# Optimization experiments

Hardware: AMD Instinct MI355X
Metric: run time of the kernel (lower is better)

The kernel has to match this reference:

```python
import jax, jax.numpy as jnp
import numpy as np

B, N, C, F, O = 32, 2048, 8, 128, 128


def setup_inputs() -> dict:
    key = jax.random.key(0)
    k1, k2, k3, k4, k5, k6 = jax.random.split(key, 6)
    nodes = jax.random.normal(k1, (B, N, F), dtype=jnp.float32)
    children = jax.random.randint(k2, (B, N, C), 0, N, dtype=jnp.int32)
    w_t = jax.random.normal(k3, (F, O), dtype=jnp.float32) * 0.05
    w_l = jax.random.normal(k4, (F, O), dtype=jnp.float32) * 0.05
    w_r = jax.random.normal(k5, (F, O), dtype=jnp.float32) * 0.05
    b = jax.random.normal(k6, (O,), dtype=jnp.float32) * 0.05
    return {"nodes": nodes, "children": children, "w_t": w_t, "w_l": w_l, "w_r": w_r, "b": b}


def reference(nodes, children, w_t, w_l, w_r, b):
    Bb, Nn, Ff = nodes.shape
    Cc = children.shape[2]
    dt = nodes.dtype

    # --- children tensor: index 0 maps to zero vector ---
    lookup = jnp.concatenate([jnp.zeros((Bb, 1, Ff), dt), nodes[:, 1:, :]], axis=1)
    batch_idx = jnp.arange(Bb)[:, None, None]
    child_vecs = lookup[batch_idx, children]                      # [B,N,C,F]
    tree = jnp.concatenate([nodes[:, :, None, :], child_vecs], axis=2)  # [B,N,C+1,F]

    # --- coefficients ---
    ch_f = children.astype(dt)
    c_t = jnp.broadcast_to(
        jnp.concatenate([jnp.ones((1, 1, 1), dt), jnp.zeros((1, 1, Cc), dt)], axis=2),
        (Bb, Nn, Cc + 1))                                          # [B,N,C+1]
    num_sib = jnp.count_nonzero(children, axis=2, keepdims=True).astype(dt)  # [B,N,1]
    mask = jnp.concatenate(
        [jnp.zeros((Bb, Nn, 1), dt), jnp.minimum(ch_f, 1.0)], axis=2)        # [B,N,C+1]
    child_indices = jnp.arange(-1.0, Cc, 1.0, dtype=dt)[None, None, :] * mask
    singles = jnp.concatenate(
        [jnp.zeros((Bb, Nn, 1), dt),
         jnp.full((Bb, Nn, 1), 0.5, dt),
         jnp.zeros((Bb, Nn, Cc - 1), dt)], axis=2)
    is_single = num_sib == 1.0
    denom = jnp.where(is_single, 1.0, num_sib - 1.0)  # safe divide, matches tf.where select
    c_r = jnp.where(is_single, singles, (1.0 - c_t) * (child_indices / denom))
    c_l = (1.0 - c_t) * (1.0 - c_r) * mask
    coef = jnp.stack([c_t, c_r, c_l], axis=3)                      # [B,N,C+1,3]

    # --- weighted aggregation + small GEMM ---
    agg = jnp.einsum('bncf,bnck->bnkf', tree, coef)                # [B,N,3,F]
    w = jnp.stack([w_t, w_r, w_l], axis=0)                         # [3,F,O]
    out = jnp.einsum('bnkf,kfo->bno', agg, w)
    return jax.nn.relu(out + b)
```

## Files before the change

kernel.cpp:

```cpp
#include <hip/hip_runtime.h>

typedef unsigned short ushort_t;
typedef __attribute__((ext_vector_type(8))) short short8;
typedef __attribute__((ext_vector_type(4))) float float4v;
typedef __attribute__((ext_vector_type(2))) unsigned int uint2v;

#define Bn 32
#define Nn 2048
#define Cn 8
#define Fn 128
#define On 128
#define Kn 384
#define MT 16
#define LDSK 392

__device__ __forceinline__ ushort_t f2bf(float x) {
  unsigned u = __float_as_uint(x);
  u += 0x7fffu + ((u >> 16) & 1u);
  return (ushort_t)(u >> 16);
}

__device__ __forceinline__ unsigned cvt_pk_bf16(float lo, float hi) {
  unsigned r;
  asm("v_cvt_pk_bf16_f32 %0, %1, %2" : "=v"(r) : "v"(lo), "v"(hi));
  return r;
}

__device__ __forceinline__ uint2v pack4(float4v v) {
  uint2v r;
  r.x = cvt_pk_bf16(v.x, v.y);
  r.y = cvt_pk_bf16(v.z, v.w);
  return r;
}

__global__ void prep_w_kernel(const float* __restrict__ w_t,
                              const float* __restrict__ w_l,
                              const float* __restrict__ w_r,
                              ushort_t* __restrict__ wsw) {
  int t = blockIdx.x * blockDim.x + threadIdx.x;
  if (t >= 6144) return;
  int lane = t & 63;
  int r = t >> 6;
  int ks = r % 12;
  int q = r / 12;
  int col = q * 16 + (lane & 15);
  int kbase = ((lane >> 4) * 8) + ks * 32;
  ushort_t* dst = wsw + (size_t)t * 8;
#pragma unroll
  for (int j = 0; j < 8; ++j) {
    int k = kbase + j;
    const float* src = (k < Fn) ? w_t : (k < 2 * Fn) ? w_r : w_l;
    int f = k & (Fn - 1);
    dst[j] = f2bf(src[f * On + col]);
  }
}

__device__ __forceinline__ void issue_row(const float* __restrict__ nodes,
                                          int sb, int grp, int ln,
                                          const int4& a, const int4& b,
                                          int it, float4v (&dst)[9]) {
  const int row = it * 4 + grp;
  const int g = sb * MT + row;
  const int base_row = g & ~(Nn - 1);
  const float4v* np = (const float4v*)nodes;
  dst[0] = np[(size_t)g * (Fn / 4) + ln];
  const int id[Cn] = {a.x, a.y, a.z, a.w, b.x, b.y, b.z, b.w};
#pragma unroll
  for (int c = 0; c < Cn; ++c) {
    const int ix = id[c] & (Nn - 1);
    dst[1 + c] = np[(size_t)(base_row + ix) * (Fn / 4) + ln];
  }
}

__device__ __forceinline__ void compute_row(ushort_t* __restrict__ agg,
                                            int grp, int ln,
                                            const int4& a, const int4& b,
                                            int it, const float4v (&v)[9]) {
  const int row = it * 4 + grp;
  const int id[Cn] = {a.x, a.y, a.z, a.w, b.x, b.y, b.z, b.w};
  int ns = 0;
#pragma unroll
  for (int c = 0; c < Cn; ++c) ns += (id[c] != 0) ? 1 : 0;
  const bool single = (ns == 1);
  const float rden = (ns > 1) ? (1.0f / (float)(ns - 1)) : 0.0f;

  float4v rr = {0.f, 0.f, 0.f, 0.f};
  float4v ms = {0.f, 0.f, 0.f, 0.f};
#pragma unroll
  for (int c = 0; c < Cn; ++c) {
    const float m = (id[c] != 0) ? 1.0f : 0.0f;
    float cr = single ? ((c == 0) ? 0.5f : 0.0f) : ((float)c * rden);
    cr *= m;
    const float4v vc = v[1 + c];
    rr += cr * vc;
    ms += m * vc;
  }
  const float4v ll = ms - rr;

  ushort_t* arow = agg + row * LDSK + ln * 4;
  *(uint2v*)(arow)           = pack4(v[0]);
  *(uint2v*)(arow + Fn)      = pack4(rr);
  *(uint2v*)(arow + 2 * Fn)  = pack4(ll);
}

__device__ __forceinline__ void store_ct(float* __restrict__ out,
                                         const float* __restrict__ bias,
                                         int sb, int l15, int quad, int q,
                                         const float4v& acc) {
  const int col = q * 16 + l15;
  const float bb = bias[col];
  const int grow0 = sb * MT + quad * 4;
#pragma unroll
  for (int r2 = 0; r2 < 4; ++r2) {
    out[(size_t)(grow0 + r2) * On + col] = fmaxf(acc[r2] + bb, 0.f);
  }
}

__global__ __launch_bounds__(128, 3)
void tree_conv_kernel(const float* __restrict__ nodes,
                      const int* __restrict__ children,
                      const ushort_t* __restrict__ wsw,
                      const float* __restrict__ bias,
                      float* __restrict__ out) {
  __shared__ __align__(16) ushort_t agg[MT * LDSK];

  const int tid = threadIdx.x;

  const int sb = ((blockIdx.x & 7) << 9) | (blockIdx.x >> 3);

  {
    const int grp = tid >> 5;
    const int ln = tid & 31;

    int4 ca[4], cb[4];
#pragma unroll
    for (int it = 0; it < 4; ++it) {
      const int g = sb * MT + it * 4 + grp;
      const int4* chv = (const int4*)(children + (size_t)g * Cn);
      ca[it] = chv[0];
      cb[it] = chv[1];
    }

    float4v v0[9], v1[9];
    issue_row(nodes, sb, grp, ln, ca[0], cb[0], 0, v0);
    issue_row(nodes, sb, grp, ln, ca[1], cb[1], 1, v1);
    compute_row(agg, grp, ln, ca[0], cb[0], 0, v0);
    issue_row(nodes, sb, grp, ln, ca[2], cb[2], 2, v0);
    compute_row(agg, grp, ln, ca[1], cb[1], 1, v1);
    issue_row(nodes, sb, grp, ln, ca[3], cb[3], 3, v1);
    compute_row(agg, grp, ln, ca[2], cb[2], 2, v0);
    compute_row(agg, grp, ln, ca[3], cb[3], 3, v1);
  }

  const int lane = tid & 63;
  const int wave = tid >> 6;
  const int l15 = lane & 15;
  const int quad = lane >> 4;

  short8 bf0[12], bf1[12];
  const short8* bbase = (const short8*)wsw + lane;
#pragma unroll
  for (int ks = 0; ks < 12; ++ks) bf0[ks] = bbase[((wave * 4 + 0) * 12 + ks) * 64];
#pragma unroll
  for (int ks = 0; ks < 12; ++ks) bf1[ks] = bbase[((wave * 4 + 1) * 12 + ks) * 64];

  asm volatile("s_waitcnt lgkmcnt(0)" ::: "memory");
  __builtin_amdgcn_s_barrier();
  asm volatile("" ::: "memory");

  const ushort_t* ar = agg + l15 * LDSK + quad * 8;
  short8 af[12];
#pragma unroll
  for (int ks = 0; ks < 12; ++ks) af[ks] = *(const short8*)(ar + ks * 32);

  float4v acc;

  acc = (float4v){0.f, 0.f, 0.f, 0.f};
#pragma unroll
  for (int ks = 0; ks < 12; ++ks)
    acc = __builtin_amdgcn_mfma_f32_16x16x32_bf16(af[ks], bf0[ks], acc, 0, 0, 0);
#pragma unroll
  for (int ks = 0; ks < 12; ++ks) bf0[ks] = bbase[((wave * 4 + 2) * 12 + ks) * 64];
  store_ct(out, bias, sb, l15, quad, wave * 4 + 0, acc);

  acc = (float4v){0.f, 0.f, 0.f, 0.f};
#pragma unroll
  for (int ks = 0; ks < 12; ++ks)
    acc = __builtin_amdgcn_mfma_f32_16x16x32_bf16(af[ks], bf1[ks], acc, 0, 0, 0);
#pragma unroll
  for (int ks = 0; ks < 12; ++ks) bf1[ks] = bbase[((wave * 4 + 3) * 12 + ks) * 64];
  store_ct(out, bias, sb, l15, quad, wave * 4 + 1, acc);

  acc = (float4v){0.f, 0.f, 0.f, 0.f};
#pragma unroll
  for (int ks = 0; ks < 12; ++ks)
    acc = __builtin_amdgcn_mfma_f32_16x16x32_bf16(af[ks], bf0[ks], acc, 0, 0, 0);
  store_ct(out, bias, sb, l15, quad, wave * 4 + 2, acc);

  acc = (float4v){0.f, 0.f, 0.f, 0.f};
#pragma unroll
  for (int ks = 0; ks < 12; ++ks)
    acc = __builtin_amdgcn_mfma_f32_16x16x32_bf16(af[ks], bf1[ks], acc, 0, 0, 0);
  store_ct(out, bias, sb, l15, quad, wave * 4 + 3, acc);
}

extern "C" void kernel_launch(void* const* d_in, const int* in_sizes, int n_in,
                              void* d_out, int out_size, void* d_ws, size_t ws_size,
                              hipStream_t stream) {
  const float* nodes = (const float*)d_in[0];
  const int* children = (const int*)d_in[1];
  const float* w_t = (const float*)d_in[2];
  const float* w_l = (const float*)d_in[3];
  const float* w_r = (const float*)d_in[4];
  const float* bias = (const float*)d_in[5];
  float* out = (float*)d_out;
  ushort_t* wsw = (ushort_t*)d_ws;

  prep_w_kernel<<<24, 256, 0, stream>>>(w_t, w_l, w_r, wsw);
  tree_conv_kernel<<<(Bn * Nn) / MT, 128, 0, stream>>>(nodes, children, wsw, bias, out);
}
```

Baseline: 119.9 us.

## Enlarge row tile to 64 with 256 threads and reuse weight fragments

```diff
diff --git a/kernel.cpp b/kernel.cpp
--- a/kernel.cpp
+++ b/kernel.cpp
@@ -11,8 +11,9 @@
 #define Fn 128
 #define On 128
 #define Kn 384
-#define MT 16
+#define MT 64
 #define LDSK 392
+#define NBLK ((Bn * Nn) / MT)
 
 __device__ __forceinline__ ushort_t f2bf(float x) {
   unsigned u = __float_as_uint(x);
@@ -56,11 +57,9 @@
 }
 
 __device__ __forceinline__ void issue_row(const float* __restrict__ nodes,
-                                          int sb, int grp, int ln,
+                                          int g, int ln,
                                           const int4& a, const int4& b,
-                                          int it, float4v (&dst)[9]) {
-  const int row = it * 4 + grp;
-  const int g = sb * MT + row;
+                                          float4v (&dst)[9]) {
   const int base_row = g & ~(Nn - 1);
   const float4v* np = (const float4v*)nodes;
   dst[0] = np[(size_t)g * (Fn / 4) + ln];
@@ -73,10 +72,9 @@
 }
 
 __device__ __forceinline__ void compute_row(ushort_t* __restrict__ agg,
-                                            int grp, int ln,
+                                            int row, int ln,
                                             const int4& a, const int4& b,
-                                            int it, const float4v (&v)[9]) {
-  const int row = it * 4 + grp;
+                                            const float4v (&v)[9]) {
   const int id[Cn] = {a.x, a.y, a.z, a.w, b.x, b.y, b.z, b.w};
   int ns = 0;
 #pragma unroll
@@ -98,25 +96,12 @@
   const float4v ll = ms - rr;
 
   ushort_t* arow = agg + row * LDSK + ln * 4;
-  *(uint2v*)(arow)           = pack4(v[0]);
-  *(uint2v*)(arow + Fn)      = pack4(rr);
-  *(uint2v*)(arow + 2 * Fn)  = pack4(ll);
-}
-
-__device__ __forceinline__ void store_ct(float* __restrict__ out,
-                                         const float* __restrict__ bias,
-                                         int sb, int l15, int quad, int q,
-                                         const float4v& acc) {
-  const int col = q * 16 + l15;
-  const float bb = bias[col];
-  const int grow0 = sb * MT + quad * 4;
-#pragma unroll
-  for (int r2 = 0; r2 < 4; ++r2) {
-    out[(size_t)(grow0 + r2) * On + col] = fmaxf(acc[r2] + bb, 0.f);
-  }
-}
-
-__global__ __launch_bounds__(128, 3)
+  *(uint2v*)(arow)          = pack4(v[0]);
+  *(uint2v*)(arow + Fn)     = pack4(rr);
+  *(uint2v*)(arow + 2 * Fn) = pack4(ll);
+}
+
+__global__ __launch_bounds__(256, 3)
 void tree_conv_kernel(const float* __restrict__ nodes,
                       const int* __restrict__ children,
                       const ushort_t* __restrict__ wsw,
@@ -126,82 +111,90 @@
 
   const int tid = threadIdx.x;
 
-  const int sb = ((blockIdx.x & 7) << 9) | (blockIdx.x >> 3);
+  const int sb = ((blockIdx.x & 7) << 7) | (blockIdx.x >> 3);
 
   {
     const int grp = tid >> 5;
     const int ln = tid & 31;
-
-    int4 ca[4], cb[4];
-#pragma unroll
-    for (int it = 0; it < 4; ++it) {
-      const int g = sb * MT + it * 4 + grp;
-      const int4* chv = (const int4*)(children + (size_t)g * Cn);
-      ca[it] = chv[0];
-      cb[it] = chv[1];
-    }
+    const int g0 = sb * MT + grp;
+
+    int4 ca[8], cb[8];
+#define LDCH(i)                                                              \
+  {                                                                          \
+    const int4* chv = (const int4*)(children + (size_t)(g0 + (i)*8) * Cn);   \
+    ca[i] = chv[0];                                                          \
+    cb[i] = chv[1];                                                          \
+  }
+    LDCH(0) LDCH(1) LDCH(2)
 
     float4v v0[9], v1[9];
-    issue_row(nodes, sb, grp, ln, ca[0], cb[0], 0, v0);
-    issue_row(nodes, sb, grp, ln, ca[1], cb[1], 1, v1);
-    compute_row(agg, grp, ln, ca[0], cb[0], 0, v0);
-    issue_row(nodes, sb, grp, ln, ca[2], cb[2], 2, v0);
-    compute_row(agg, grp, ln, ca[1], cb[1], 1, v1);
-    issue_row(nodes, sb, grp, ln, ca[3], cb[3], 3, v1);
-    compute_row(agg, grp, ln, ca[2], cb[2], 2, v0);
-    compute_row(agg, grp, ln, ca[3], cb[3], 3, v1);
+    issue_row(nodes, g0 + 0 * 8, ln, ca[0], cb[0], v0);
+    LDCH(3)
+    issue_row(nodes, g0 + 1 * 8, ln, ca[1], cb[1], v1);
+    compute_row(agg, 0 * 8 + grp, ln, ca[0], cb[0], v0);
+    LDCH(4)
+    issue_row(nodes, g0 + 2 * 8, ln, ca[2], cb[2], v0);
+    compute_row(agg, 1 * 8 + grp, ln, ca[1], cb[1], v1);
+    LDCH(5)
+    issue_row(nodes, g0 + 3 * 8, ln, ca[3], cb[3], v1);
+    compute_row(agg, 2 * 8 + grp, ln, ca[2], cb[2], v0);
+    LDCH(6)
+    issue_row(nodes, g0 + 4 * 8, ln, ca[4], cb[4], v0);
+    compute_row(agg, 3 * 8 + grp, ln, ca[3], cb[3], v1);
+    LDCH(7)
+    issue_row(nodes, g0 + 5 * 8, ln, ca[5], cb[5], v1);
+    compute_row(agg, 4 * 8 + grp, ln, ca[4], cb[4], v0);
+    issue_row(nodes, g0 + 6 * 8, ln, ca[6], cb[6], v0);
+    compute_row(agg, 5 * 8 + grp, ln, ca[5], cb[5], v1);
+    issue_row(nodes, g0 + 7 * 8, ln, ca[7], cb[7], v1);
+    compute_row(agg, 6 * 8 + grp, ln, ca[6], cb[6], v0);
+    compute_row(agg, 7 * 8 + grp, ln, ca[7], cb[7], v1);
+#undef LDCH
   }
 
   const int lane = tid & 63;
   const int wave = tid >> 6;
   const int l15 = lane & 15;
   const int quad = lane >> 4;
+  const int ct0 = wave * 2, ct1 = wave * 2 + 1;
 
   short8 bf0[12], bf1[12];
   const short8* bbase = (const short8*)wsw + lane;
 #pragma unroll
-  for (int ks = 0; ks < 12; ++ks) bf0[ks] = bbase[((wave * 4 + 0) * 12 + ks) * 64];
-#pragma unroll
-  for (int ks = 0; ks < 12; ++ks) bf1[ks] = bbase[((wave * 4 + 1) * 12 + ks) * 64];
+  for (int ks = 0; ks < 12; ++ks) bf0[ks] = bbase[(ct0 * 12 + ks) * 64];
+#pragma unroll
+  for (int ks = 0; ks < 12; ++ks) bf1[ks] = bbase[(ct1 * 12 + ks) * 64];
+  const float bb0 = bias[ct0 * 16 + l15];
+  const float bb1 = bias[ct1 * 16 + l15];
 
   asm volatile("s_waitcnt lgkmcnt(0)" ::: "memory");
   __builtin_amdgcn_s_barrier();
   asm volatile("" ::: "memory");
 
-  const ushort_t* ar = agg + l15 * LDSK + quad * 8;
-  short8 af[12];
-#pragma unroll
-  for (int ks = 0; ks < 12; ++ks) af[ks] = *(const short8*)(ar + ks * 32);
-
-  float4v acc;
-
-  acc = (float4v){0.f, 0.f, 0.f, 0.f};
-#pragma unroll
-  for (int ks = 0; ks < 12; ++ks)
-    acc = __builtin_amdgcn_mfma_f32_16x16x32_bf16(af[ks], bf0[ks], acc, 0, 0, 0);
-#pragma unroll
-  for (int ks = 0; ks < 12; ++ks) bf0[ks] = bbase[((wave * 4 + 2) * 12 + ks) * 64];
-  store_ct(out, bias, sb, l15, quad, wave * 4 + 0, acc);
-
-  acc = (float4v){0.f, 0.f, 0.f, 0.f};
-#pragma unroll
-  for (int ks = 0; ks < 12; ++ks)
-    acc = __builtin_amdgcn_mfma_f32_16x16x32_bf16(af[ks], bf1[ks], acc, 0, 0, 0);
-#pragma unroll
-  for (int ks = 0; ks < 12; ++ks) bf1[ks] = bbase[((wave * 4 + 3) * 12 + ks) * 64];
-  store_ct(out, bias, sb, l15, quad, wave * 4 + 1, acc);
-
-  acc = (float4v){0.f, 0.f, 0.f, 0.f};
-#pragma unroll
-  for (int ks = 0; ks < 12; ++ks)
-    acc = __builtin_amdgcn_mfma_f32_16x16x32_bf16(af[ks], bf0[ks], acc, 0, 0, 0);
-  store_ct(out, bias, sb, l15, quad, wave * 4 + 2, acc);
-
-  acc = (float4v){0.f, 0.f, 0.f, 0.f};
-#pragma unroll
-  for (int ks = 0; ks < 12; ++ks)
-    acc = __builtin_amdgcn_mfma_f32_16x16x32_bf16(af[ks], bf1[ks], acc, 0, 0, 0);
-  store_ct(out, bias, sb, l15, quad, wave * 4 + 3, acc);
+#pragma unroll
+  for (int mt = 0; mt < 4; ++mt) {
+    const ushort_t* ar = agg + (mt * 16 + l15) * LDSK + quad * 8;
+    short8 af[12];
+#pragma unroll
+    for (int ks = 0; ks < 12; ++ks) af[ks] = *(const short8*)(ar + ks * 32);
+
+    float4v acc0 = {0.f, 0.f, 0.f, 0.f};
+    float4v acc1 = {0.f, 0.f, 0.f, 0.f};
+#pragma unroll
+    for (int ks = 0; ks < 12; ++ks)
+      acc0 = __builtin_amdgcn_mfma_f32_16x16x32_bf16(af[ks], bf0[ks], acc0, 0, 0, 0);
+#pragma unroll
+    for (int ks = 0; ks < 12; ++ks)
+      acc1 = __builtin_amdgcn_mfma_f32_16x16x32_bf16(af[ks], bf1[ks], acc1, 0, 0, 0);
+
+    const int grow0 = sb * MT + mt * 16 + quad * 4;
+#pragma unroll
+    for (int r2 = 0; r2 < 4; ++r2) {
+      const size_t ro = (size_t)(grow0 + r2) * On;
+      out[ro + ct0 * 16 + l15] = fmaxf(acc0[r2] + bb0, 0.f);
+      out[ro + ct1 * 16 + l15] = fmaxf(acc1[r2] + bb1, 0.f);
+    }
+  }
 }
 
 extern "C" void kernel_launch(void* const* d_in, const int* in_sizes, int n_in,
@@ -217,5 +210,5 @@
   ushort_t* wsw = (ushort_t*)d_ws;
 
   prep_w_kernel<<<24, 256, 0, stream>>>(w_t, w_l, w_r, wsw);
-  tree_conv_kernel<<<(Bn * Nn) / MT, 128, 0, stream>>>(nodes, children, wsw, bias, out);
-}
+  tree_conv_kernel<<<NBLK, 256, 0, stream>>>(nodes, children, wsw, bias, out);
+}
```

Result: faster. 111.9 us (-6.6%).
